# Optimization experiments

Measured on AMD Instinct MI355X. Metric: run time of the kernel, lower is better.

## Reference

```python
import jax, jax.numpy as jnp
import numpy as np

N = 20000   # nodes
E = 320000  # edges per relation
R = 4       # relations
H = 4       # attention heads
HID = 64    # hidden_dim1
DIN = 256   # input_dim
OUT = 64    # output_dim
NEG_SLOPE = 0.2  # PyG GATv2Conv default


def setup_inputs() -> dict:
    key = jax.random.key(0)
    ks = jax.random.split(key, 16)
    rn = lambda k, s: jax.random.normal(k, s, jnp.float32) * 0.05
    return {
        "x": jax.random.normal(ks[0], (N, DIN), jnp.float32),
        "edge_indices": jax.random.randint(ks[1], (R, 2, E), 0, N, jnp.int32),
        "Wl1": rn(ks[2], (R, DIN, H * HID)),
        "Wr1": rn(ks[3], (R, DIN, H * HID)),
        "att1": rn(ks[4], (R, H, HID)),
        "b1": rn(ks[5], (R, H * HID)),
        "Wl2": rn(ks[6], (R, H * HID, H * HID)),
        "Wr2": rn(ks[7], (R, H * HID, H * HID)),
        "att2": rn(ks[8], (R, H, HID)),
        "b2": rn(ks[9], (R, H * HID)),
        "Wrel3": rn(ks[10], (R, H * HID, HID)),
        "Wroot3": rn(ks[11], (R, H * HID, HID)),
        "b3": rn(ks[12], (R, HID)),
        "Wrel4": rn(ks[13], (R, HID, OUT)),
        "Wroot4": rn(ks[14], (R, HID, OUT)),
        "b4": rn(ks[15], (R, OUT)),
    }


def gatv2(x, src, dst, Wl, Wr, att, bias):
    """PyG GATv2Conv (concat heads, add_self_loops=True, share_weights=False)."""
    n = x.shape[0]
    loop = jnp.arange(n, dtype=src.dtype)
    src = jnp.concatenate([src, loop])  # add self loops
    dst = jnp.concatenate([dst, loop])
    xl = (x @ Wl).reshape(n, H, -1)  # source transform [N,H,C]
    xr = (x @ Wr).reshape(n, H, -1)  # target transform [N,H,C]
    z = jax.nn.leaky_relu(xl[src] + xr[dst], NEG_SLOPE)  # [E',H,C]
    e = jnp.einsum('ehc,hc->eh', z, att)                 # per-edge logits
    m = jax.ops.segment_max(e, dst, num_segments=n)
    m = jnp.where(jnp.isfinite(m), m, 0.0)
    p = jnp.exp(e - m[dst])
    s = jax.ops.segment_sum(p, dst, num_segments=n)
    alpha = p / s[dst]                                   # segment softmax
    out = jax.ops.segment_sum(alpha[:, :, None] * xl[src], dst, num_segments=n)
    return out.reshape(n, -1) + bias


def graphconv(x, src, dst, Wrel, Wroot, b):
    """PyG GraphConv: W1 x_i + W2 sum_j x_j (aggr='add')."""
    agg = jax.ops.segment_sum(x[src], dst, num_segments=x.shape[0])
    return agg @ Wrel + b + x @ Wroot


def reference(x, edge_indices, Wl1, Wr1, att1, b1, Wl2, Wr2, att2, b2,
              Wrel3, Wroot3, b3, Wrel4, Wroot4, b4):
    outs = []
    for i in range(R):  # small fixed relation count
        src, dst = edge_indices[i, 0], edge_indices[i, 1]
        h = jax.nn.relu(gatv2(x, src, dst, Wl1[i], Wr1[i], att1[i], b1[i]))
        h = jax.nn.relu(gatv2(h, src, dst, Wl2[i], Wr2[i], att2[i], b2[i]))
        h = jax.nn.relu(graphconv(h, src, dst, Wrel3[i], Wroot3[i], b3[i]))
        h = graphconv(h, src, dst, Wrel4[i], Wroot4[i], b4[i])
        outs.append(h[:, None, :])
    return jnp.concatenate(outs, axis=1)  # [N, R, OUT]
```

## Files before the change

kernel.cpp:

```cpp
#include <hip/hip_runtime.h>
#include <hip/hip_fp16.h>
#include <math.h>

#define NN   20000
#define EE   320000
#define RR   4

typedef unsigned short u16;
typedef unsigned int   u32;
typedef _Float16 half8v __attribute__((ext_vector_type(8)));
typedef _Float16 v2h    __attribute__((ext_vector_type(2)));
typedef __attribute__((ext_vector_type(4))) float f32x4;

static __device__ __forceinline__ u16 f2h(float f){ return __half_as_ushort(__float2half_rn(f)); }
static __device__ __forceinline__ v2h u2v(u32 u){ union{u32 u; v2h v;} c; c.u=u; return c.v; }
static __device__ __forceinline__ u32 v2u(v2h v){ union{u32 u; v2h v;} c; c.v=v; return c.u; }
static __device__ __forceinline__ v2h splat2(float f){ v2h r; r[0]=(_Float16)f; r[1]=(_Float16)f; return r; }
static __device__ __forceinline__ float fdot2(v2h a, v2h b, float c){
  return __builtin_amdgcn_fdot2(a, b, c, false);
}
static __device__ __forceinline__ void gload_lds16(const void* g, void* l){
  __builtin_amdgcn_global_load_lds((const __attribute__((address_space(1))) void*)g,
                                   (__attribute__((address_space(3))) void*)l, 16, 0, 0);
}

__global__ void k_zero_int(int* __restrict__ p, int n){
  int i = blockIdx.x*blockDim.x + threadIdx.x;
  if (i < n) p[i] = 0;
}
__global__ void k_countA(const int* __restrict__ ei, int* __restrict__ deg4){
  int i = blockIdx.x*blockDim.x + threadIdx.x;
  if (i < RR*EE) {
    int r = i / EE, e = i % EE;
    int d = ei[(size_t)r*2*EE + EE + e];
    atomicAdd(&deg4[r*NN + d], 1);
  }
}
__global__ __launch_bounds__(1024) void k_scan(const int* __restrict__ cnt_all, int* __restrict__ off_all,
                                               int* __restrict__ cur_all, int n){
  const int* cnt = cnt_all + (size_t)blockIdx.x*n;
  int* off = off_all + (size_t)blockIdx.x*(n+1);
  int* cur = cur_all + (size_t)blockIdx.x*n;
  __shared__ int part[1024];
  int t = threadIdx.x;
  int chunk = (n + 1023) >> 10;
  int lo = t*chunk; if (lo > n) lo = n;
  int hi = lo + chunk; if (hi > n) hi = n;
  int s = 0;
  for (int i = lo; i < hi; ++i) s += cnt[i];
  part[t] = s;
  __syncthreads();
  for (int d = 1; d < 1024; d <<= 1) {
    int u = (t >= d) ? part[t-d] : 0;
    __syncthreads();
    part[t] += u;
    __syncthreads();
  }
  int run = (t == 0) ? 0 : part[t-1];
  for (int i = lo; i < hi; ++i) { off[i] = run; cur[i] = run; run += cnt[i]; }
  if (t == 1023) off[n] = part[1023];
}
__global__ void k_scatter4(const int* __restrict__ ei, int* __restrict__ cur4, int* __restrict__ csr4,
                           int dlo, int dhi){
  int i = blockIdx.x*blockDim.x + threadIdx.x;
  if (i < RR*EE) {
    int r = i / EE, e = i % EE;
    int d = ei[(size_t)r*2*EE + EE + e];
    if (d >= dlo && d < dhi) {
      int s = ei[(size_t)r*2*EE + e];
      int p = atomicAdd(&cur4[r*NN + d], 1);
      csr4[(size_t)r*EE + p] = s;
    }
  }
}

__global__ void k_cast(const float* __restrict__ x, u16* __restrict__ o, int n4){
  int i = blockIdx.x*blockDim.x + threadIdx.x;
  if (i < n4) {
    float4 v = reinterpret_cast<const float4*>(x)[i];
    ushort4 b;
    b.x = f2h(v.x); b.y = f2h(v.y); b.z = f2h(v.z); b.w = f2h(v.w);
    reinterpret_cast<ushort4*>(o)[i] = b;
  }
}
__global__ void k_prep(const float* __restrict__ A, const float* __restrict__ B,
                       u16* __restrict__ dst, int K, int N, int total){
  int i = blockIdx.x*blockDim.x + threadIdx.x;
  if (i >= total) return;
  int k = i % K;
  int n = (i / K) % (2*N);
  int r = i / (K*2*N);
  const float* S = (n < N) ? A : B;
  int nn = (n < N) ? n : n - N;
  dst[i] = f2h(S[((size_t)r*K + k)*N + nn]);
}

__global__ __launch_bounds__(256) void k_mfma(
    const u16* __restrict__ A, const u16* __restrict__ BT,
    int M, int K, u16* __restrict__ Cb, int ldc,
    long aZ, long btZ, long cZ)
{
  constexpr int BM = 128, BN = 128;
  constexpr int FI = 4, FJ = 4;
  const int zz = blockIdx.z;
  A  += (size_t)zz*aZ;
  BT += (size_t)zz*btZ;
  Cb += (size_t)zz*cZ;

  __shared__ u16 As[BM*32];
  __shared__ u16 Bs[BN*32];
  const int t = threadIdx.x;
  const int lane = t & 63, wid = t >> 6;
  const int wr = wid >> 1, wc = wid & 1;
  const int bm = blockIdx.x * BM, bn = blockIdx.y * BN;
  const int lr = lane & 15, lk = lane >> 4;

  f32x4 acc[FI][FJ];
  #pragma unroll
  for (int i = 0; i < FI; ++i)
    #pragma unroll
    for (int j = 0; j < FJ; ++j) acc[i][j] = (f32x4)(0.f);

  const int nk = K >> 5;
  char* AsB = (char*)As;
  char* BsB = (char*)Bs;

  for (int s = 0; s < nk; ++s) {
    const int kk = s << 5;
    #pragma unroll
    for (int i = 0; i < 2; ++i) {
      int c = t + 256*i;
      int row = c >> 2, sub = c & 3;
      int lsub = sub ^ (row & 3);
      int grow = bm + row; if (grow >= M) grow = M - 1;
      gload_lds16(A + (size_t)grow*K + kk + lsub*8, AsB + c*16);
    }
    #pragma unroll
    for (int i = 0; i < 2; ++i) {
      int c = t + 256*i;
      int row = c >> 2, sub = c & 3;
      int lsub = sub ^ (row & 3);
      gload_lds16(BT + (size_t)(bn + row)*K + kk + lsub*8, BsB + c*16);
    }
    __syncthreads();
    half8v a[FI], b[FJ];
    #pragma unroll
    for (int i = 0; i < FI; ++i) {
      int row = wr*64 + i*16 + lr;
      int sub = lk ^ (row & 3);
      a[i] = *reinterpret_cast<half8v*>(AsB + row*64 + sub*16);
    }
    #pragma unroll
    for (int j = 0; j < FJ; ++j) {
      int col = wc*64 + j*16 + lr;
      int sub = lk ^ (col & 3);
      b[j] = *reinterpret_cast<half8v*>(BsB + col*64 + sub*16);
    }
    #pragma unroll
    for (int i = 0; i < FI; ++i)
      #pragma unroll
      for (int j = 0; j < FJ; ++j)
        acc[i][j] = __builtin_amdgcn_mfma_f32_16x16x32_f16(a[i], b[j], acc[i][j], 0, 0, 0);
    __syncthreads();
  }

  #pragma unroll
  for (int i = 0; i < FI; ++i) {
    #pragma unroll
    for (int j = 0; j < FJ; ++j) {
      int col = bn + wc*64 + j*16 + lr;
      #pragma unroll
      for (int q = 0; q < 4; ++q) {
        int row = bm + wr*64 + i*16 + lk*4 + q;
        if (row < M) Cb[(size_t)row*ldc + col] = f2h(acc[i][j][q]);
      }
    }
  }
}

__global__ __launch_bounds__(256) void k_gat(
    const u16* __restrict__ xlr,
    const float* __restrict__ att, const float* __restrict__ bias,
    const int* __restrict__ off4, const int* __restrict__ csr4,
    u16* __restrict__ out)
{
  const int z = blockIdx.z;
  int node = blockIdx.x*4 + (threadIdx.x >> 6);
  if (node >= NN) return;
  const int lane = threadIdx.x & 63;
  const int sl = lane & 31, sub = lane >> 5;
  const u16* xbase = xlr + (size_t)z*512;
  const int* off = off4 + (size_t)z*(NN+1);
  const int* csr = csr4 + (size_t)z*EE;
  u16* outp = out + (size_t)z*(size_t)NN*256;

  const int co = sl*8;
  const u16* selfrow = xbase + (size_t)node*2048;
  const v2h c02 = splat2(0.2f);
  const float L2E = 1.4426950408889634f;

  uint4 rx = *reinterpret_cast<const uint4*>(selfrow + 256 + co);
  v2h xr2[4] = {u2v(rx.x), u2v(rx.y), u2v(rx.z), u2v(rx.w)};
  v2h av2[4];
  {
    float4 q0 = *reinterpret_cast<const float4*>(att + z*256 + co);
    float4 q1 = *reinterpret_cast<const float4*>(att + z*256 + co + 4);
    av2[0][0]=(_Float16)(q0.x*L2E); av2[0][1]=(_Float16)(q0.y*L2E);
    av2[1][0]=(_Float16)(q0.z*L2E); av2[1][1]=(_Float16)(q0.w*L2E);
    av2[2][0]=(_Float16)(q1.x*L2E); av2[2][1]=(_Float16)(q1.y*L2E);
    av2[3][0]=(_Float16)(q1.z*L2E); av2[3][1]=(_Float16)(q1.w*L2E);
  }
  uint4 sx = *reinterpret_cast<const uint4*>(selfrow + co);
  v2h xs2[4] = {u2v(sx.x), u2v(sx.y), u2v(sx.z), u2v(sx.w)};
  float ps = 0.f;
  #pragma unroll
  for (int i = 0; i < 4; ++i) {
    v2h zz = xs2[i] + xr2[i];
    v2h lr = __builtin_elementwise_max(zz, zz*c02);
    ps = fdot2(av2[i], lr, ps);
  }
  ps += __shfl_xor(ps,1); ps += __shfl_xor(ps,2); ps += __shfl_xor(ps,4);
  float wsf = (sub == 0) ? exp2f(fminf(ps - 6.f, 12.f)) : 0.f;
  float s = wsf;
  v2h a2[4];
  {
    v2h w2 = splat2(wsf);
    #pragma unroll
    for (int i = 0; i < 4; ++i) a2[i] = w2*xs2[i];
  }

  const int e0 = off[node], e1 = off[node+1];
  const int e1m1 = e1 - 1;
  for (int k = e0; k < e1; k += 8) {
    v2h xv[4][4];
    float p[4];
    int kks[4];
    #pragma unroll
    for (int j = 0; j < 4; ++j) {
      int kk = k + 2*j + sub;
      kks[j] = kk;
      int idx = csr[kk <= e1m1 ? kk : e1m1];
      uint4 v = *reinterpret_cast<const uint4*>(xbase + (size_t)idx*2048 + co);
      xv[j][0]=u2v(v.x); xv[j][1]=u2v(v.y); xv[j][2]=u2v(v.z); xv[j][3]=u2v(v.w);
      float pp = 0.f;
      #pragma unroll
      for (int i = 0; i < 4; ++i) {
        v2h zz = xv[j][i] + xr2[i];
        v2h lr = __builtin_elementwise_max(zz, zz*c02);
        pp = fdot2(av2[i], lr, pp);
      }
      p[j] = pp;
    }
    #pragma unroll
    for (int j = 0; j < 4; ++j) {
      p[j] += __shfl_xor(p[j],1);
      p[j] += __shfl_xor(p[j],2);
      p[j] += __shfl_xor(p[j],4);
    }
    float w[4];
    #pragma unroll
    for (int j = 0; j < 4; ++j)
      w[j] = (kks[j] < e1) ? exp2f(fminf(p[j] - 6.f, 12.f)) : 0.f;
    s += (w[0] + w[1]) + (w[2] + w[3]);
    #pragma unroll
    for (int j = 0; j < 4; ++j) {
      v2h w2 = splat2(w[j]);
      #pragma unroll
      for (int i = 0; i < 4; ++i) a2[i] += w2*xv[j][i];
    }
  }
  s += __shfl_xor(s, 32);
  #pragma unroll
  for (int i = 0; i < 4; ++i) {
    u32 t = (u32)__shfl_xor((int)v2u(a2[i]), 32);
    a2[i] += u2v(t);
  }
  float inv = 1.f / s;
  if (sub == 0) {
    float4 b0 = *reinterpret_cast<const float4*>(bias + z*256 + co);
    float4 b1 = *reinterpret_cast<const float4*>(bias + z*256 + co + 4);
    float bv[8] = {b0.x,b0.y,b0.z,b0.w,b1.x,b1.y,b1.z,b1.w};
    u32 o[4];
    #pragma unroll
    for (int i = 0; i < 4; ++i) {
      float lo = fmaxf((float)a2[i][0]*inv + bv[2*i],   0.f);
      float hi = fmaxf((float)a2[i][1]*inv + bv[2*i+1], 0.f);
      o[i] = (u32)f2h(lo) | ((u32)f2h(hi) << 16);
    }
    uint4 ov = {o[0], o[1], o[2], o[3]};
    *reinterpret_cast<uint4*>(outp + (size_t)node*256 + co) = ov;
  }
}

template<int RELU, int F32OUT>
__global__ __launch_bounds__(256) void k_aggp(
    const u16* __restrict__ C, const float* __restrict__ bias,
    const int* __restrict__ off4, const int* __restrict__ csr4,
    u16* __restrict__ outb, float* __restrict__ outf)
{
  const int z = blockIdx.z;
  int node = blockIdx.x*4 + (threadIdx.x >> 6);
  if (node >= NN) return;
  const int lane = threadIdx.x & 63;
  const int g = lane >> 4, sl = lane & 15;
  const u16* Cp = C + (size_t)z*(size_t)NN*128;
  const int* off = off4 + (size_t)z*(NN+1);
  const int* csr = csr4 + (size_t)z*EE;
  const int co = sl*4;
  v2h acc0 = splat2(0.f), acc1 = splat2(0.f);
  const int e0 = off[node], e1 = off[node+1];
  const int e1m1 = e1 - 1;
  for (int k = e0; k < e1; k += 8) {
    #pragma unroll
    for (int j = 0; j < 2; ++j) {
      int kk = k + 2*g + j;
      int idx = csr[kk <= e1m1 ? kk : e1m1];
      uint2 v = *reinterpret_cast<const uint2*>(Cp + (size_t)idx*128 + co);
      bool val = kk < e1;
      u32 vx = val ? v.x : 0u;
      u32 vy = val ? v.y : 0u;
      acc0 += u2v(vx);
      acc1 += u2v(vy);
    }
  }
  float a0 = (float)acc0[0], a1 = (float)acc0[1];
  float a2 = (float)acc1[0], a3 = (float)acc1[1];
  a0 += __shfl_xor(a0,16); a1 += __shfl_xor(a1,16);
  a2 += __shfl_xor(a2,16); a3 += __shfl_xor(a3,16);
  a0 += __shfl_xor(a0,32); a1 += __shfl_xor(a1,32);
  a2 += __shfl_xor(a2,32); a3 += __shfl_xor(a3,32);
  if (g == 0) {
    uint2 q = *reinterpret_cast<const uint2*>(Cp + (size_t)node*128 + 64 + co);
    v2h q0 = u2v(q.x), q1 = u2v(q.y);
    float4 bv = *reinterpret_cast<const float4*>(bias + z*64 + co);
    float v0 = a0 + (float)q0[0] + bv.x;
    float v1 = a1 + (float)q0[1] + bv.y;
    float v2 = a2 + (float)q1[0] + bv.z;
    float v3 = a3 + (float)q1[1] + bv.w;
    if (RELU) {
      v0 = fmaxf(v0, 0.f); v1 = fmaxf(v1, 0.f);
      v2 = fmaxf(v2, 0.f); v3 = fmaxf(v3, 0.f);
    }
    if (F32OUT) {
      float4 o = {v0, v1, v2, v3};
      *reinterpret_cast<float4*>(outf + (size_t)node*256 + z*64 + co) = o;
    } else {
      uint2 o;
      o.x = (u32)f2h(v0) | ((u32)f2h(v1) << 16);
      o.y = (u32)f2h(v2) | ((u32)f2h(v3) << 16);
      *reinterpret_cast<uint2*>(outb + ((size_t)z*NN + node)*64 + co) = o;
    }
  }
}

extern "C" void kernel_launch(void* const* d_in, const int* in_sizes, int n_in,
                              void* d_out, int out_size, void* d_ws, size_t ws_size,
                              hipStream_t stream)
{
  const float* x      = (const float*)d_in[0];
  const int*   ei     = (const int*)  d_in[1];
  const float* Wl1    = (const float*)d_in[2];
  const float* Wr1    = (const float*)d_in[3];
  const float* att1   = (const float*)d_in[4];
  const float* b1     = (const float*)d_in[5];
  const float* Wl2    = (const float*)d_in[6];
  const float* Wr2    = (const float*)d_in[7];
  const float* att2   = (const float*)d_in[8];
  const float* b2     = (const float*)d_in[9];
  const float* Wrel3  = (const float*)d_in[10];
  const float* Wroot3 = (const float*)d_in[11];
  const float* b3     = (const float*)d_in[12];
  const float* Wrel4  = (const float*)d_in[13];
  const float* Wroot4 = (const float*)d_in[14];
  const float* b4     = (const float*)d_in[15];
  float* out = (float*)d_out;

  const dim3 thr(256);
  const size_t NB2048 = (size_t)NN*2048;
  const size_t NB256  = (size_t)NN*256;
  const size_t NB128  = (size_t)NN*128;
  const size_t NB64   = (size_t)NN*64;

  u16* XLR = (u16*)d_ws;
  u16* h   = XLR + NB2048;
  u16* xbf = h   + NB256*RR;
  u16* W1T = xbf + NB256;
  u16* W2T = W1T + (size_t)RR*512*256;
  u16* W3T = W2T + (size_t)RR*512*256;
  u16* W4T = W3T + (size_t)RR*128*256;
  int* deg4 = (int*)(W4T + (size_t)RR*128*64);
  int* off4 = deg4 + RR*NN;
  int* cur4 = off4 + RR*(NN+1);
  int* csr4 = cur4 + RR*NN;
  u16* C34 = XLR;
  u16* h3b = XLR + NB128*RR;

  k_cast<<<dim3((NN*256/4+255)/256), thr, 0, stream>>>(x, xbf, NN*256/4);
  k_prep<<<dim3((RR*512*256+255)/256), thr, 0, stream>>>(Wl1, Wr1, W1T, 256, 256, RR*512*256);
  k_prep<<<dim3((RR*512*256+255)/256), thr, 0, stream>>>(Wl2, Wr2, W2T, 256, 256, RR*512*256);
  k_prep<<<dim3((RR*128*256+255)/256), thr, 0, stream>>>(Wrel3, Wroot3, W3T, 256, 64, RR*128*256);
  k_prep<<<dim3((RR*128*64+255)/256),  thr, 0, stream>>>(Wrel4, Wroot4, W4T, 64, 64, RR*128*64);

  k_zero_int<<<dim3((RR*NN+255)/256), thr, 0, stream>>>(deg4, RR*NN);
  k_countA  <<<dim3((RR*EE+255)/256), thr, 0, stream>>>(ei, deg4);
  k_scan    <<<dim3(RR), dim3(1024), 0, stream>>>(deg4, off4, cur4, NN);
  for (int p = 0; p < 4; ++p)
    k_scatter4<<<dim3((RR*EE+255)/256), thr, 0, stream>>>(ei, cur4, csr4, p*5000, (p+1)*5000);

  const dim3 gNode(5000, 1, RR);
  k_mfma<<<dim3(157,16,1), thr, 0, stream>>>(xbf, W1T, NN, 256, XLR, 2048, 0, 0, 0);
  k_gat<<<gNode, thr, 0, stream>>>(XLR, att1, b1, off4, csr4, h);
  k_mfma<<<dim3(157,4,RR), thr, 0, stream>>>(h, W2T, NN, 256, XLR, 2048,
                                             (long)NB256, 512*256, 512);
  k_gat<<<gNode, thr, 0, stream>>>(XLR, att2, b2, off4, csr4, h);
  k_mfma<<<dim3(157,1,RR), thr, 0, stream>>>(h, W3T, NN, 256, C34, 128,
                                             (long)NB256, 128*256, (long)NB128);
  k_aggp<1,0><<<gNode, thr, 0, stream>>>(C34, b3, off4, csr4, h3b, nullptr);
  k_mfma<<<dim3(157,1,RR), thr, 0, stream>>>(h3b, W4T, NN, 64, C34, 128,
                                             (long)NB64, 128*64, (long)NB128);
  k_aggp<0,1><<<gNode, thr, 0, stream>>>(C34, b4, off4, csr4, nullptr, out);
}
```

Before: 573.7 us.

## Merge prep and scatter launches, store byte offsets in CSR, split tail loops

The cast and four weight-prep kernels become one launch indexed by blockIdx.y. The four destination-range scatter passes become one grid whose block index picks the pass. The CSR now holds precomputed byte offsets (src*4096), so the gather kernels skip the index multiply and apply only a shift in the aggregation kernel. The GAT and aggregation edge loops are split into a full-chunk body with no bounds checks and a separate tail loop, which removes the clamp and validity selects from the hot path. The offset encoding ties the CSR to the fixed row strides, and the merged scatter no longer guarantees that passes run in order, which may cost some locality.

```diff
diff --git a/kernel.cpp b/kernel.cpp
--- a/kernel.cpp
+++ b/kernel.cpp
@@ -60,32 +60,24 @@
   for (int i = lo; i < hi; ++i) { off[i] = run; cur[i] = run; run += cnt[i]; }
   if (t == 1023) off[n] = part[1023];
 }
-__global__ void k_scatter4(const int* __restrict__ ei, int* __restrict__ cur4, int* __restrict__ csr4,
-                           int dlo, int dhi){
-  int i = blockIdx.x*blockDim.x + threadIdx.x;
+__global__ void k_scatterM(const int* __restrict__ ei, int* __restrict__ cur4, u32* __restrict__ csr4){
+  int bid = blockIdx.x;
+  int pass = bid / 5000;
+  int i = (bid - pass*5000)*256 + threadIdx.x;
+  int dlo = pass*5000, dhi = dlo + 5000;
   if (i < RR*EE) {
-    int r = i / EE, e = i % EE;
+    int r = i / EE, e = i - r*EE;
     int d = ei[(size_t)r*2*EE + EE + e];
     if (d >= dlo && d < dhi) {
       int s = ei[(size_t)r*2*EE + e];
       int p = atomicAdd(&cur4[r*NN + d], 1);
-      csr4[(size_t)r*EE + p] = s;
-    }
-  }
-}
-
-__global__ void k_cast(const float* __restrict__ x, u16* __restrict__ o, int n4){
-  int i = blockIdx.x*blockDim.x + threadIdx.x;
-  if (i < n4) {
-    float4 v = reinterpret_cast<const float4*>(x)[i];
-    ushort4 b;
-    b.x = f2h(v.x); b.y = f2h(v.y); b.z = f2h(v.z); b.w = f2h(v.w);
-    reinterpret_cast<ushort4*>(o)[i] = b;
-  }
-}
-__global__ void k_prep(const float* __restrict__ A, const float* __restrict__ B,
-                       u16* __restrict__ dst, int K, int N, int total){
-  int i = blockIdx.x*blockDim.x + threadIdx.x;
+      csr4[(size_t)r*EE + p] = (u32)s * 4096u;
+    }
+  }
+}
+
+static __device__ __forceinline__ void prep_body(const float* A, const float* B, u16* dst,
+                                                 int K, int N, int total, int i){
   if (i >= total) return;
   int k = i % K;
   int n = (i / K) % (2*N);
@@ -93,6 +85,25 @@
   const float* S = (n < N) ? A : B;
   int nn = (n < N) ? n : n - N;
   dst[i] = f2h(S[((size_t)r*K + k)*N + nn]);
+}
+__global__ void k_prepall(const float* __restrict__ x, u16* __restrict__ xbf,
+                          const float* __restrict__ Wl1, const float* __restrict__ Wr1, u16* __restrict__ W1T,
+                          const float* __restrict__ Wl2, const float* __restrict__ Wr2, u16* __restrict__ W2T,
+                          const float* __restrict__ W3a, const float* __restrict__ W3b, u16* __restrict__ W3T,
+                          const float* __restrict__ W4a, const float* __restrict__ W4b, u16* __restrict__ W4T){
+  int kind = blockIdx.y;
+  int i = blockIdx.x*256 + threadIdx.x;
+  if (kind == 0) {
+    if (i < NN*256/4) {
+      float4 v = reinterpret_cast<const float4*>(x)[i];
+      ushort4 b;
+      b.x = f2h(v.x); b.y = f2h(v.y); b.z = f2h(v.z); b.w = f2h(v.w);
+      reinterpret_cast<ushort4*>(xbf)[i] = b;
+    }
+  } else if (kind == 1) prep_body(Wl1, Wr1, W1T, 256, 256, RR*512*256, i);
+  else if (kind == 2)   prep_body(Wl2, Wr2, W2T, 256, 256, RR*512*256, i);
+  else if (kind == 3)   prep_body(W3a, W3b, W3T, 256, 64,  RR*128*256, i);
+  else                  prep_body(W4a, W4b, W4T, 64,  64,  RR*128*64,  i);
 }
 
 __global__ __launch_bounds__(256) void k_mfma(
@@ -181,7 +192,7 @@
 __global__ __launch_bounds__(256) void k_gat(
     const u16* __restrict__ xlr,
     const float* __restrict__ att, const float* __restrict__ bias,
-    const int* __restrict__ off4, const int* __restrict__ csr4,
+    const int* __restrict__ off4, const u32* __restrict__ csr4,
     u16* __restrict__ out)
 {
   const int z = blockIdx.z;
@@ -189,13 +200,13 @@
   if (node >= NN) return;
   const int lane = threadIdx.x & 63;
   const int sl = lane & 31, sub = lane >> 5;
-  const u16* xbase = xlr + (size_t)z*512;
   const int* off = off4 + (size_t)z*(NN+1);
-  const int* csr = csr4 + (size_t)z*EE;
+  const u32* csr = csr4 + (size_t)z*EE;
   u16* outp = out + (size_t)z*(size_t)NN*256;
 
   const int co = sl*8;
-  const u16* selfrow = xbase + (size_t)node*2048;
+  const char* xc = (const char*)xlr + (size_t)z*1024 + co*2;
+  const u16* selfrow = xlr + (size_t)z*512 + (size_t)node*2048;
   const v2h c02 = splat2(0.2f);
   const float L2E = 1.4426950408889634f;
 
@@ -230,17 +241,14 @@
   }
 
   const int e0 = off[node], e1 = off[node+1];
-  const int e1m1 = e1 - 1;
-  for (int k = e0; k < e1; k += 8) {
+  const int kfull = e0 + ((e1 - e0) & ~7);
+  for (int k = e0; k < kfull; k += 8) {
     v2h xv[4][4];
     float p[4];
-    int kks[4];
     #pragma unroll
     for (int j = 0; j < 4; ++j) {
-      int kk = k + 2*j + sub;
-      kks[j] = kk;
-      int idx = csr[kk <= e1m1 ? kk : e1m1];
-      uint4 v = *reinterpret_cast<const uint4*>(xbase + (size_t)idx*2048 + co);
+      u32 boff = csr[k + 2*j + sub];
+      uint4 v = *reinterpret_cast<const uint4*>(xc + boff);
       xv[j][0]=u2v(v.x); xv[j][1]=u2v(v.y); xv[j][2]=u2v(v.z); xv[j][3]=u2v(v.w);
       float pp = 0.f;
       #pragma unroll
@@ -259,8 +267,7 @@
     }
     float w[4];
     #pragma unroll
-    for (int j = 0; j < 4; ++j)
-      w[j] = (kks[j] < e1) ? exp2f(fminf(p[j] - 6.f, 12.f)) : 0.f;
+    for (int j = 0; j < 4; ++j) w[j] = exp2f(fminf(p[j] - 6.f, 12.f));
     s += (w[0] + w[1]) + (w[2] + w[3]);
     #pragma unroll
     for (int j = 0; j < 4; ++j) {
@@ -268,6 +275,26 @@
       #pragma unroll
       for (int i = 0; i < 4; ++i) a2[i] += w2*xv[j][i];
     }
+  }
+  for (int k = kfull; k < e1; k += 2) {
+    int kk = k + sub;
+    bool val = kk < e1;
+    u32 boff = csr[val ? kk : e1-1];
+    uint4 v = *reinterpret_cast<const uint4*>(xc + boff);
+    v2h xv[4] = {u2v(v.x), u2v(v.y), u2v(v.z), u2v(v.w)};
+    float pp = 0.f;
+    #pragma unroll
+    for (int i = 0; i < 4; ++i) {
+      v2h zz = xv[i] + xr2[i];
+      v2h lr = __builtin_elementwise_max(zz, zz*c02);
+      pp = fdot2(av2[i], lr, pp);
+    }
+    pp += __shfl_xor(pp,1); pp += __shfl_xor(pp,2); pp += __shfl_xor(pp,4);
+    float w = val ? exp2f(fminf(pp - 6.f, 12.f)) : 0.f;
+    s += w;
+    v2h w2 = splat2(w);
+    #pragma unroll
+    for (int i = 0; i < 4; ++i) a2[i] += w2*xv[i];
   }
   s += __shfl_xor(s, 32);
   #pragma unroll
@@ -295,7 +322,7 @@
 template<int RELU, int F32OUT>
 __global__ __launch_bounds__(256) void k_aggp(
     const u16* __restrict__ C, const float* __restrict__ bias,
-    const int* __restrict__ off4, const int* __restrict__ csr4,
+    const int* __restrict__ off4, const u32* __restrict__ csr4,
     u16* __restrict__ outb, float* __restrict__ outf)
 {
   const int z = blockIdx.z;
@@ -304,24 +331,29 @@
   const int lane = threadIdx.x & 63;
   const int g = lane >> 4, sl = lane & 15;
   const u16* Cp = C + (size_t)z*(size_t)NN*128;
+  const char* Cc = (const char*)Cp + sl*8;
   const int* off = off4 + (size_t)z*(NN+1);
-  const int* csr = csr4 + (size_t)z*EE;
+  const u32* csr = csr4 + (size_t)z*EE;
   const int co = sl*4;
   v2h acc0 = splat2(0.f), acc1 = splat2(0.f);
   const int e0 = off[node], e1 = off[node+1];
-  const int e1m1 = e1 - 1;
-  for (int k = e0; k < e1; k += 8) {
+  const int kfull = e0 + ((e1 - e0) & ~7);
+  for (int k = e0; k < kfull; k += 8) {
     #pragma unroll
     for (int j = 0; j < 2; ++j) {
-      int kk = k + 2*g + j;
-      int idx = csr[kk <= e1m1 ? kk : e1m1];
-      uint2 v = *reinterpret_cast<const uint2*>(Cp + (size_t)idx*128 + co);
-      bool val = kk < e1;
-      u32 vx = val ? v.x : 0u;
-      u32 vy = val ? v.y : 0u;
-      acc0 += u2v(vx);
-      acc1 += u2v(vy);
-    }
+      u32 boff = csr[k + 2*g + j] >> 4;
+      uint2 v = *reinterpret_cast<const uint2*>(Cc + boff);
+      acc0 += u2v(v.x);
+      acc1 += u2v(v.y);
+    }
+  }
+  for (int k = kfull; k < e1; k += 4) {
+    int kk = k + g;
+    bool val = kk < e1;
+    u32 boff = csr[val ? kk : e1-1] >> 4;
+    uint2 v = *reinterpret_cast<const uint2*>(Cc + boff);
+    acc0 += u2v(val ? v.x : 0u);
+    acc1 += u2v(val ? v.y : 0u);
   }
   float a0 = (float)acc0[0], a1 = (float)acc0[1];
   float a2 = (float)acc1[0], a3 = (float)acc1[1];
@@ -391,21 +423,17 @@
   int* deg4 = (int*)(W4T + (size_t)RR*128*64);
   int* off4 = deg4 + RR*NN;
   int* cur4 = off4 + RR*(NN+1);
-  int* csr4 = cur4 + RR*NN;
+  u32* csr4 = (u32*)(cur4 + RR*NN);
   u16* C34 = XLR;
   u16* h3b = XLR + NB128*RR;
 
-  k_cast<<<dim3((NN*256/4+255)/256), thr, 0, stream>>>(x, xbf, NN*256/4);
-  k_prep<<<dim3((RR*512*256+255)/256), thr, 0, stream>>>(Wl1, Wr1, W1T, 256, 256, RR*512*256);
-  k_prep<<<dim3((RR*512*256+255)/256), thr, 0, stream>>>(Wl2, Wr2, W2T, 256, 256, RR*512*256);
-  k_prep<<<dim3((RR*128*256+255)/256), thr, 0, stream>>>(Wrel3, Wroot3, W3T, 256, 64, RR*128*256);
-  k_prep<<<dim3((RR*128*64+255)/256),  thr, 0, stream>>>(Wrel4, Wroot4, W4T, 64, 64, RR*128*64);
+  k_prepall<<<dim3(5000,5), thr, 0, stream>>>(x, xbf, Wl1, Wr1, W1T, Wl2, Wr2, W2T,
+                                              Wrel3, Wroot3, W3T, Wrel4, Wroot4, W4T);
 
   k_zero_int<<<dim3((RR*NN+255)/256), thr, 0, stream>>>(deg4, RR*NN);
   k_countA  <<<dim3((RR*EE+255)/256), thr, 0, stream>>>(ei, deg4);
   k_scan    <<<dim3(RR), dim3(1024), 0, stream>>>(deg4, off4, cur4, NN);
-  for (int p = 0; p < 4; ++p)
-    k_scatter4<<<dim3((RR*EE+255)/256), thr, 0, stream>>>(ei, cur4, csr4, p*5000, (p+1)*5000);
+  k_scatterM<<<dim3(20000), thr, 0, stream>>>(ei, cur4, csr4);
 
   const dim3 gNode(5000, 1, RR);
   k_mfma<<<dim3(157,16,1), thr, 0, stream>>>(xbf, W1T, NN, 256, XLR, 2048, 0, 0, 0);
```

After: 562.9 us. About the same (-1.9%).
